# Kernel tuning notes

Measured on AMD Instinct MI355X. Metric: run time of the kernel, lower is better.

## Reference

```python
import jax, jax.numpy as jnp
import numpy as np

B, L, D, H = 4, 1024, 1024, 16
DK = D // H


def setup_inputs() -> dict:
    key = jax.random.key(0)
    ks = jax.random.split(key, 5)
    s = 1.0 / np.sqrt(D)  # roughly nn.Linear init scale
    return {
        "x": jax.random.normal(ks[0], (B, L, D), dtype=jnp.float32),
        "Wq": jax.random.normal(ks[1], (D, D), dtype=jnp.float32) * s,
        "bq": jnp.zeros((D,), dtype=jnp.float32),
        "Wk": jax.random.normal(ks[2], (D, D), dtype=jnp.float32) * s,
        "bk": jnp.zeros((D,), dtype=jnp.float32),
        "Wv": jax.random.normal(ks[3], (D, D), dtype=jnp.float32) * s,
        "bv": jnp.zeros((D,), dtype=jnp.float32),
        "Wo": jax.random.normal(ks[4], (D, D), dtype=jnp.float32) * s,
        "bo": jnp.zeros((D,), dtype=jnp.float32),
    }


def reference(x, Wq, bq, Wk, bk, Wv, bv, Wo, bo):
    b, l, d = x.shape
    # torch Linear: y = x @ W.T + b
    q = (x @ Wq.T + bq).reshape(b, l, H, DK).transpose(0, 2, 1, 3)  # [B,H,L,DK]
    k = (x @ Wk.T + bk).reshape(b, l, H, DK).transpose(0, 2, 1, 3)
    v = (x @ Wv.T + bv).reshape(b, l, H, DK).transpose(0, 2, 1, 3)
    scores = jnp.einsum("bhqd,bhkd->bhqk", q, k) / jnp.sqrt(jnp.float32(DK))
    attn = jax.nn.softmax(scores, axis=-1)  # dropout p=0 -> identity
    head_out = jnp.einsum("bhqk,bhkd->bhqd", attn, v)  # [B,H,L,DK]
    merged = head_out.transpose(0, 2, 1, 3).reshape(b, l, d)  # [B,L,D]
    out = merged @ Wo.T + bo
    # DeCov loss over head outputs
    U = merged.reshape(b * l, d)
    U = U - U.mean(axis=0, keepdims=True)
    C = (U.T @ U) / jnp.float32(b * l)
    decov = 0.5 * (jnp.sum(C * C) - jnp.sum(jnp.diag(C) ** 2))
    return (out, decov)
```

## Files before the change

### kernel.cpp

```cpp
#include <hip/hip_runtime.h>
#include <cstdint>
#include <cstddef>

typedef short v4s __attribute__((ext_vector_type(4)));
typedef short v8s __attribute__((ext_vector_type(8)));
typedef float v4f __attribute__((ext_vector_type(4)));

__device__ __forceinline__ short f2bf(float f) {
    union { float f; unsigned u; } x; x.f = f;
    unsigned r = (x.u + 0x7FFFu + ((x.u >> 16) & 1u)) >> 16;
    return (short)(unsigned short)r;
}
__device__ __forceinline__ float bf2f(short h) {
    union { unsigned u; float f; } x; x.u = ((unsigned)(unsigned short)h) << 16;
    return x.f;
}

__device__ __forceinline__ void gld16(const void* g, void* l) {
    __builtin_amdgcn_global_load_lds((const __attribute__((address_space(1))) void*)g,
                                     (__attribute__((address_space(3))) void*)l, 16, 0, 0);
}

__global__ __launch_bounds__(256) void cvt_bf16(
    const float* __restrict__ x, const float* __restrict__ wq, const float* __restrict__ wk,
    const float* __restrict__ wv, const float* __restrict__ wo,
    short* __restrict__ xb, short* __restrict__ wqb, short* __restrict__ wkb,
    short* __restrict__ wvb, short* __restrict__ wob, float* __restrict__ colsum,
    float* __restrict__ dtot, int* __restrict__ dcnt)
{
    int bid = blockIdx.x;
    const float* src; short* dst; size_t base;
    if (bid < 4096)      { src = x;  dst = xb;  base = (size_t)bid * 1024; }
    else if (bid < 5120) { src = wq; dst = wqb; base = (size_t)(bid - 4096) * 1024; }
    else if (bid < 6144) { src = wk; dst = wkb; base = (size_t)(bid - 5120) * 1024; }
    else if (bid < 7168) { src = wv; dst = wvb; base = (size_t)(bid - 6144) * 1024; }
    else                 { src = wo; dst = wob; base = (size_t)(bid - 7168) * 1024; }
    size_t idx = base + (size_t)threadIdx.x * 4;
    v4f v = *(const v4f*)(src + idx);
    v4s o;
    o[0] = f2bf(v[0]); o[1] = f2bf(v[1]); o[2] = f2bf(v[2]); o[3] = f2bf(v[3]);
    *(v4s*)(dst + idx) = o;
    if (bid == 0) {
        v4f z = {0.f, 0.f, 0.f, 0.f};
        *(v4f*)(colsum + (size_t)threadIdx.x * 4) = z;
        if (threadIdx.x == 0) { *dtot = 0.f; *dcnt = 0; }
    }
}

__global__ __launch_bounds__(256) void gemm_qkv(
    const short* __restrict__ xb,
    const short* __restrict__ wq, const short* __restrict__ wk, const short* __restrict__ wv,
    const float* __restrict__ bq, const float* __restrict__ bk, const float* __restrict__ bv,
    short* __restrict__ qo, short* __restrict__ ko, short* __restrict__ vto)
{
    __shared__ __align__(16) short At[128 * 32];
    __shared__ __align__(16) short Bt[128 * 32];
    const int K = 1024;
    const int mode = blockIdx.z;
    const short* W = (mode == 0) ? wq : (mode == 1) ? wk : wv;
    const float* bias = (mode == 0) ? bq : (mode == 1) ? bk : bv;
    const int m0 = blockIdx.y * 128, n0 = blockIdx.x * 128;
    const int tid = threadIdx.x, wave = tid >> 6, lane = tid & 63;
    const int quad = lane >> 4, ll = lane & 15;
    const int wr = wave >> 1, wc = wave & 1;
    const v4f zero4 = {0.f, 0.f, 0.f, 0.f};
    v4f acc[4][4];
    for (int i = 0; i < 4; ++i) for (int j = 0; j < 4; ++j) acc[i][j] = zero4;

    for (int k0 = 0; k0 < K; k0 += 32) {
        __syncthreads();
#pragma unroll
        for (int c = 0; c < 2; ++c) {
            int chb = (wave * 2 + c) * 64;
            int ch = chb + lane;
            int row = ch >> 2, col8 = (ch & 3) * 8;
            gld16(xb + (size_t)(m0 + row) * K + k0 + col8, &At[chb * 8]);
            gld16(W  + (size_t)(n0 + row) * K + k0 + col8, &Bt[chb * 8]);
        }
        __syncthreads();
        v8s af[4], bfr[4];
#pragma unroll
        for (int i = 0; i < 4; ++i) af[i]  = *(const v8s*)&At[(wr * 64 + i * 16 + ll) * 32 + quad * 8];
#pragma unroll
        for (int j = 0; j < 4; ++j) bfr[j] = *(const v8s*)&Bt[(wc * 64 + j * 16 + ll) * 32 + quad * 8];
#pragma unroll
        for (int i = 0; i < 4; ++i)
#pragma unroll
            for (int j = 0; j < 4; ++j)
                acc[i][j] = __builtin_amdgcn_mfma_f32_16x16x32_bf16(af[i], bfr[j], acc[i][j], 0, 0, 0);
    }

    const float scale = (mode == 0) ? 0.125f : 1.0f;
#pragma unroll
    for (int j = 0; j < 4; ++j) {
        int n = n0 + wc * 64 + j * 16 + ll;
        float bb = bias[n];
        int hh = n >> 6, dk = n & 63;
#pragma unroll
        for (int i = 0; i < 4; ++i) {
            int mbase = m0 + wr * 64 + i * 16 + quad * 4;
#pragma unroll
            for (int r = 0; r < 4; ++r) {
                int m = mbase + r;
                int b = m >> 10, li = m & 1023;
                short h = f2bf((acc[i][j][r] + bb) * scale);
                if (mode == 0)
                    qo[(((size_t)(b * 16 + hh) * 1024 + li) << 6) + dk] = h;
                else if (mode == 1)
                    ko[(((size_t)(b * 16 + hh) * 1024 + li) << 6) + dk] = h;
                else
                    vto[(((size_t)(b * 16 + hh) * 64 + dk) << 10) + li] = h;
            }
        }
    }
}

__global__ __launch_bounds__(256) void attn_flash(
    const short* __restrict__ qb, const short* __restrict__ kb, const short* __restrict__ vtb,
    float* __restrict__ merged, short* __restrict__ mergedh, float* __restrict__ colsum)
{
    __shared__ __align__(16) short Kt[64 * 64];
    __shared__ __align__(16) short Vt[64 * 64];
    __shared__ __align__(16) short Pt[4 * 32 * 68];
    const int bh = blockIdx.y, qt = blockIdx.x;
    const int tid = threadIdx.x, wave = tid >> 6, lane = tid & 63;
    const int quad = lane >> 4, ll = lane & 15;
    const short* qp = qb  + (size_t)bh * 1024 * 64;
    const short* kp = kb  + (size_t)bh * 1024 * 64;
    const short* vp = vtb + (size_t)bh * 64 * 1024;

    v8s qa[2][2];
#pragma unroll
    for (int mi = 0; mi < 2; ++mi) {
        int qrow = qt * 128 + wave * 32 + mi * 16 + ll;
        qa[mi][0] = *(const v8s*)(qp + (size_t)qrow * 64 + quad * 8);
        qa[mi][1] = *(const v8s*)(qp + (size_t)qrow * 64 + 32 + quad * 8);
    }

    const v4f zero4 = {0.f, 0.f, 0.f, 0.f};
    v4f oacc[2][4];
    for (int mi = 0; mi < 2; ++mi) for (int nt = 0; nt < 4; ++nt) oacc[mi][nt] = zero4;
    float lsum[2][4];
    for (int mi = 0; mi < 2; ++mi) for (int r = 0; r < 4; ++r) lsum[mi][r] = 0.f;
    short* pw = &Pt[wave * 32 * 68];

    for (int jt = 0; jt < 16; ++jt) {
        __syncthreads();
#pragma unroll
        for (int c = 0; c < 2; ++c) {
            int chb = (wave * 2 + c) * 64;
            int ch = chb + lane;
            int row = ch >> 3;
            int gi = ((ch & 7) ^ (row & 7)) * 8;
            gld16(kp + (size_t)(jt * 64 + row) * 64 + gi, &Kt[chb * 8]);
            gld16(vp + (size_t)row * 1024 + jt * 64 + gi, &Vt[chb * 8]);
        }
        __syncthreads();

        v4f sacc[2][4];
#pragma unroll
        for (int nt = 0; nt < 4; ++nt) {
            int n = nt * 16 + ll;
            int g0 = (quad ^ (n & 7)) * 8;
            int g1 = ((4 + quad) ^ (n & 7)) * 8;
            v8s b0 = *(const v8s*)&Kt[n * 64 + g0];
            v8s b1 = *(const v8s*)&Kt[n * 64 + g1];
#pragma unroll
            for (int mi = 0; mi < 2; ++mi) {
                v4f s = zero4;
                s = __builtin_amdgcn_mfma_f32_16x16x32_bf16(qa[mi][0], b0, s, 0, 0, 0);
                s = __builtin_amdgcn_mfma_f32_16x16x32_bf16(qa[mi][1], b1, s, 0, 0, 0);
                sacc[mi][nt] = s;
            }
        }
#pragma unroll
        for (int mi = 0; mi < 2; ++mi)
#pragma unroll
            for (int nt = 0; nt < 4; ++nt)
#pragma unroll
                for (int r = 0; r < 4; ++r) {
                    float e = __expf(sacc[mi][nt][r]);
                    lsum[mi][r] += e;
                    pw[(mi * 16 + quad * 4 + r) * 68 + nt * 16 + ll] = f2bf(e);
                }
        v8s pa[2][2];
#pragma unroll
        for (int mi = 0; mi < 2; ++mi) {
            v4s p00 = *(const v4s*)&pw[(mi * 16 + ll) * 68 + quad * 8];
            v4s p01 = *(const v4s*)&pw[(mi * 16 + ll) * 68 + quad * 8 + 4];
            v4s p10 = *(const v4s*)&pw[(mi * 16 + ll) * 68 + 32 + quad * 8];
            v4s p11 = *(const v4s*)&pw[(mi * 16 + ll) * 68 + 32 + quad * 8 + 4];
            pa[mi][0] = __builtin_shufflevector(p00, p01, 0, 1, 2, 3, 4, 5, 6, 7);
            pa[mi][1] = __builtin_shufflevector(p10, p11, 0, 1, 2, 3, 4, 5, 6, 7);
        }
#pragma unroll
        for (int nt = 0; nt < 4; ++nt) {
            int n = nt * 16 + ll;
            int g0 = (quad ^ (n & 7)) * 8;
            int g1 = ((4 + quad) ^ (n & 7)) * 8;
            v8s v0 = *(const v8s*)&Vt[n * 64 + g0];
            v8s v1 = *(const v8s*)&Vt[n * 64 + g1];
#pragma unroll
            for (int mi = 0; mi < 2; ++mi) {
                oacc[mi][nt] = __builtin_amdgcn_mfma_f32_16x16x32_bf16(pa[mi][0], v0, oacc[mi][nt], 0, 0, 0);
                oacc[mi][nt] = __builtin_amdgcn_mfma_f32_16x16x32_bf16(pa[mi][1], v1, oacc[mi][nt], 0, 0, 0);
            }
        }
    }

    const int b = bh >> 4, h = bh & 15;
    float csum[4] = {0.f, 0.f, 0.f, 0.f};
#pragma unroll
    for (int mi = 0; mi < 2; ++mi) {
        float linv[4];
#pragma unroll
        for (int r = 0; r < 4; ++r) {
            float s = lsum[mi][r];
            s += __shfl_xor(s, 1); s += __shfl_xor(s, 2);
            s += __shfl_xor(s, 4); s += __shfl_xor(s, 8);
            linv[r] = 1.0f / s;
        }
#pragma unroll
        for (int r = 0; r < 4; ++r) {
            int li = qt * 128 + wave * 32 + mi * 16 + quad * 4 + r;
            size_t rowoff = ((size_t)(b * 1024 + li)) * 1024 + h * 64;
#pragma unroll
            for (int nt = 0; nt < 4; ++nt) {
                int d = nt * 16 + ll;
                float v = oacc[mi][nt][r] * linv[r];
                merged[rowoff + d] = v;
                mergedh[rowoff + d] = f2bf(v);
                csum[nt] += v;
            }
        }
    }
#pragma unroll
    for (int nt = 0; nt < 4; ++nt) {
        csum[nt] += __shfl_xor(csum[nt], 16);
        csum[nt] += __shfl_xor(csum[nt], 32);
    }
    if (quad == 0) {
#pragma unroll
        for (int nt = 0; nt < 4; ++nt)
            atomicAdd(&colsum[h * 64 + nt * 16 + ll], csum[nt]);
    }
}

__global__ __launch_bounds__(256) void post_attn(
    const short* __restrict__ A, const short* __restrict__ W, const float* __restrict__ bias,
    float* __restrict__ out,
    const float* __restrict__ merged, const float* __restrict__ colsum,
    short* __restrict__ uth, short* __restrict__ utl)
{
    __shared__ __align__(16) char smem[18432];
    const int bid = blockIdx.x;
    const int tid = threadIdx.x;
    if (bid < 256) {
        short* At = (short*)smem;
        short* Bt = (short*)(smem + 8192);
        const int K = 1024;
        const int n0 = (bid & 7) * 128, m0 = (bid >> 3) * 128;
        const int wave = tid >> 6, lane = tid & 63;
        const int quad = lane >> 4, ll = lane & 15;
        const int wr = wave >> 1, wc = wave & 1;
        const v4f zero4 = {0.f, 0.f, 0.f, 0.f};
        v4f acc[4][4];
        for (int i = 0; i < 4; ++i) for (int j = 0; j < 4; ++j) acc[i][j] = zero4;

        for (int k0 = 0; k0 < K; k0 += 32) {
            __syncthreads();
#pragma unroll
            for (int c = 0; c < 2; ++c) {
                int chb = (wave * 2 + c) * 64;
                int ch = chb + lane;
                int row = ch >> 2, col8 = (ch & 3) * 8;
                gld16(A + (size_t)(m0 + row) * K + k0 + col8, &At[chb * 8]);
                gld16(W + (size_t)(n0 + row) * K + k0 + col8, &Bt[chb * 8]);
            }
            __syncthreads();
            v8s af[4], bfr[4];
#pragma unroll
            for (int i = 0; i < 4; ++i) af[i]  = *(const v8s*)&At[(wr * 64 + i * 16 + ll) * 32 + quad * 8];
#pragma unroll
            for (int j = 0; j < 4; ++j) bfr[j] = *(const v8s*)&Bt[(wc * 64 + j * 16 + ll) * 32 + quad * 8];
#pragma unroll
            for (int i = 0; i < 4; ++i)
#pragma unroll
                for (int j = 0; j < 4; ++j)
                    acc[i][j] = __builtin_amdgcn_mfma_f32_16x16x32_bf16(af[i], bfr[j], acc[i][j], 0, 0, 0);
        }

#pragma unroll
        for (int j = 0; j < 4; ++j) {
            int n = n0 + wc * 64 + j * 16 + ll;
            float bb = bias[n];
#pragma unroll
            for (int i = 0; i < 4; ++i) {
                int mbase = m0 + wr * 64 + i * 16 + quad * 4;
#pragma unroll
                for (int r = 0; r < 4; ++r) {
                    int m = mbase + r;
                    out[(size_t)m * 1024 + n] = acc[i][j][r] + bb;
                }
            }
        }
    } else {
        short (*Hh)[72] = (short(*)[72])smem;
        short (*Hl)[72] = (short(*)[72])(smem + 9216);
        const int cid = bid - 256;
        const int d0 = (cid & 15) * 64, m0 = (cid >> 4) * 64;
        const int r0 = tid >> 4, c4 = (tid & 15) * 4;
        float mu[4];
#pragma unroll
        for (int e = 0; e < 4; ++e) mu[e] = colsum[d0 + c4 + e] * (1.0f / 4096.0f);
        for (int rr = 0; rr < 64; rr += 16) {
            int m = m0 + rr + r0;
            v4f v = *(const v4f*)(merged + (size_t)m * 1024 + d0 + c4);
#pragma unroll
            for (int e = 0; e < 4; ++e) {
                float u = v[e] - mu[e];
                short h = f2bf(u);
                Hh[c4 + e][rr + r0] = h;
                Hl[c4 + e][rr + r0] = f2bf(u - bf2f(h));
            }
        }
        __syncthreads();
        const int d = tid >> 2, mg = (tid & 3) * 16;
        v8s a0, a1, b0, b1;
#pragma unroll
        for (int e = 0; e < 8; ++e) {
            a0[e] = Hh[d][mg + e]; a1[e] = Hh[d][mg + 8 + e];
            b0[e] = Hl[d][mg + e]; b1[e] = Hl[d][mg + 8 + e];
        }
        size_t off = (size_t)(d0 + d) * 4096 + m0 + mg;
        *(v8s*)(uth + off) = a0; *(v8s*)(uth + off + 8) = a1;
        *(v8s*)(utl + off) = b0; *(v8s*)(utl + off + 8) = b1;
    }
}

__global__ __launch_bounds__(256) void gemm_decov(
    const short* __restrict__ uth, const short* __restrict__ utl, float* __restrict__ cpart)
{
    int p = blockIdx.x, I = 0, rem = p;
    while (rem >= 8 - I) { rem -= 8 - I; ++I; }
    const int J = I + rem;
    const int kbase = blockIdx.y * 256;
    __shared__ __align__(16) short Ah[128 * 32], Al[128 * 32], Bh[128 * 32], Bl[128 * 32];
    const int tid = threadIdx.x;
    const int wave = tid >> 6, lane = tid & 63;
    const int quad = lane >> 4, ll = lane & 15;
    const int wr = wave >> 1, wc = wave & 1;
    const v4f zero4 = {0.f, 0.f, 0.f, 0.f};
    v4f acc[4][4];
    for (int i = 0; i < 4; ++i) for (int j = 0; j < 4; ++j) acc[i][j] = zero4;

    short* sarr = (wave == 0) ? Ah : (wave == 1) ? Al : (wave == 2) ? Bh : Bl;
    const short* gsrc = (wave & 1) ? utl : uth;
    const int rbase = ((wave < 2) ? I : J) * 128;
    const int srow = lane >> 2, scol = (lane & 3) * 8;

    for (int kk = 0; kk < 256; kk += 32) {
        int k0 = kbase + kk;
        __syncthreads();
#pragma unroll
        for (int c = 0; c < 8; ++c) {
            int row = c * 16 + srow;
            gld16(gsrc + (size_t)(rbase + row) * 4096 + k0 + scol, &sarr[c * 512]);
        }
        __syncthreads();
        v8s bh[4], bl[4];
#pragma unroll
        for (int j = 0; j < 4; ++j) {
            int ro = (wc * 64 + j * 16 + ll) * 32 + quad * 8;
            bh[j] = *(const v8s*)&Bh[ro];
            bl[j] = *(const v8s*)&Bl[ro];
        }
#pragma unroll
        for (int i = 0; i < 4; ++i) {
            int ro = (wr * 64 + i * 16 + ll) * 32 + quad * 8;
            v8s ah = *(const v8s*)&Ah[ro];
            v8s al = *(const v8s*)&Al[ro];
#pragma unroll
            for (int j = 0; j < 4; ++j) {
                acc[i][j] = __builtin_amdgcn_mfma_f32_16x16x32_bf16(ah, bh[j], acc[i][j], 0, 0, 0);
                acc[i][j] = __builtin_amdgcn_mfma_f32_16x16x32_bf16(ah, bl[j], acc[i][j], 0, 0, 0);
                acc[i][j] = __builtin_amdgcn_mfma_f32_16x16x32_bf16(al, bh[j], acc[i][j], 0, 0, 0);
            }
        }
    }

    float* dst = cpart + ((size_t)blockIdx.y * 36 + p) * 16384;
#pragma unroll
    for (int i = 0; i < 4; ++i)
#pragma unroll
        for (int j = 0; j < 4; ++j)
#pragma unroll
            for (int r = 0; r < 4; ++r) {
                int gi2 = wr * 64 + i * 16 + quad * 4 + r;
                int gj2 = wc * 64 + j * 16 + ll;
                dst[gi2 * 128 + gj2] = acc[i][j][r];
            }
}

__global__ __launch_bounds__(256) void decov_reduce(
    const float* __restrict__ cpart, float* __restrict__ dtot, int* __restrict__ dcnt,
    float* __restrict__ out)
{
    int p = blockIdx.x, I = 0, rem = p;
    while (rem >= 8 - I) { rem -= 8 - I; ++I; }
    const int J = I + rem;
    const int t = threadIdx.x;
    const int ebase = blockIdx.y * 4096;
    __shared__ float wsums[4];
    float s = 0.f;
#pragma unroll
    for (int it = 0; it < 4; ++it) {
        int e4 = ebase + it * 1024 + t * 4;
        v4f c = {0.f, 0.f, 0.f, 0.f};
#pragma unroll
        for (int kc = 0; kc < 16; ++kc)
            c += *(const v4f*)&cpart[((size_t)kc * 36 + p) * 16384 + e4];
        int gi = I * 128 + (e4 >> 7), colb = J * 128 + (e4 & 127);
#pragma unroll
        for (int k = 0; k < 4; ++k) {
            float cv = c[k];
            if (gi != colb + k) s += cv * cv;
        }
    }
    if (I < J) s *= 2.f;
    s += __shfl_xor(s, 1); s += __shfl_xor(s, 2); s += __shfl_xor(s, 4);
    s += __shfl_xor(s, 8); s += __shfl_xor(s, 16); s += __shfl_xor(s, 32);
    if ((t & 63) == 0) wsums[t >> 6] = s;
    __syncthreads();
    if (t == 0) {
        float blk = wsums[0] + wsums[1] + wsums[2] + wsums[3];
        float o = atomicAdd(dtot, blk);
        int old = atomicAdd(dcnt, 1 + (int)(o * 0.0f));
        if (old == 143) {
            float tot = atomicAdd(dtot, 0.0f);
            out[4194304] = 0.5f * tot / (4096.0f * 4096.0f);
        }
    }
}

extern "C" void kernel_launch(void* const* d_in, const int* in_sizes, int n_in,
                              void* d_out, int out_size, void* d_ws, size_t ws_size,
                              hipStream_t stream) {
    const float* x  = (const float*)d_in[0];
    const float* Wq = (const float*)d_in[1];
    const float* bq = (const float*)d_in[2];
    const float* Wk = (const float*)d_in[3];
    const float* bk = (const float*)d_in[4];
    const float* Wv = (const float*)d_in[5];
    const float* bv = (const float*)d_in[6];
    const float* Wo = (const float*)d_in[7];
    const float* bo = (const float*)d_in[8];
    float* out = (float*)d_out;
    char* ws = (char*)d_ws;
    const size_t MB = 1ull << 20;
    short* xb      = (short*)(ws);
    short* wqb     = (short*)(ws + 8  * MB);
    short* wkb     = (short*)(ws + 10 * MB);
    short* wvb     = (short*)(ws + 12 * MB);
    short* wob     = (short*)(ws + 14 * MB);
    short* qb      = (short*)(ws + 16 * MB);
    short* kb      = (short*)(ws + 24 * MB);
    short* vtb     = (short*)(ws + 32 * MB);
    float* merged  = (float*)(ws + 40 * MB);
    short* mergedh = (short*)(ws + 56 * MB);
    short* uth     = (short*)(ws + 65 * MB);
    short* utl     = (short*)(ws + 73 * MB);
    float* dtot    = (float*)(ws + 81 * MB);
    int*   dcnt    = (int*)(ws + 81 * MB + 64);
    float* colsum  = (float*)(ws + 81 * MB + 4096);
    float* cpart   = (float*)(ws);

    hipLaunchKernelGGL(cvt_bf16, dim3(8192), dim3(256), 0, stream,
                       x, Wq, Wk, Wv, Wo, xb, wqb, wkb, wvb, wob, colsum, dtot, dcnt);
    hipLaunchKernelGGL(gemm_qkv, dim3(8, 32, 3), dim3(256), 0, stream,
                       xb, wqb, wkb, wvb, bq, bk, bv, qb, kb, vtb);
    hipLaunchKernelGGL(attn_flash, dim3(8, 64), dim3(256), 0, stream,
                       qb, kb, vtb, merged, mergedh, colsum);
    hipLaunchKernelGGL(post_attn, dim3(1280), dim3(256), 0, stream,
                       mergedh, wob, bo, out, merged, colsum, uth, utl);
    hipLaunchKernelGGL(gemm_decov, dim3(36, 16), dim3(256), 0, stream, uth, utl, cpart);
    hipLaunchKernelGGL(decov_reduce, dim3(36, 4), dim3(256), 0, stream, cpart, dtot, dcnt, out);
}
```

Measured before the change: 241.0 us.

## Load two K/V tiles per barrier pair, use exp2, and swap attention grid order

The attention kernel now stages two 64-key K/V tiles per iteration, which halves the number of __syncthreads pairs and issues more global loads before each wait. The log2(e) factor is folded into the Q scale in the QKV GEMM so the softmax can call exp2f instead of __expf. The grid axes are swapped so consecutive blocks cover different heads rather than different query tiles of the same head, which changes L2 locality. Shared memory use doubles for K/V, which may reduce occupancy.

New measurement: 239.2 us. No clear change (-0.7%).

```diff
diff --git a/kernel.cpp b/kernel.cpp
--- a/kernel.cpp
+++ b/kernel.cpp
@@ -90,7 +90,7 @@
                 acc[i][j] = __builtin_amdgcn_mfma_f32_16x16x32_bf16(af[i], bfr[j], acc[i][j], 0, 0, 0);
     }
 
-    const float scale = (mode == 0) ? 0.125f : 1.0f;
+    const float scale = (mode == 0) ? 0.125f * 1.44269504f : 1.0f;
 #pragma unroll
     for (int j = 0; j < 4; ++j) {
         int n = n0 + wc * 64 + j * 16 + ll;
@@ -119,10 +119,10 @@
     const short* __restrict__ qb, const short* __restrict__ kb, const short* __restrict__ vtb,
     float* __restrict__ merged, short* __restrict__ mergedh, float* __restrict__ colsum)
 {
-    __shared__ __align__(16) short Kt[64 * 64];
-    __shared__ __align__(16) short Vt[64 * 64];
+    __shared__ __align__(16) short Kt[2 * 64 * 64];
+    __shared__ __align__(16) short Vt[2 * 64 * 64];
     __shared__ __align__(16) short Pt[4 * 32 * 68];
-    const int bh = blockIdx.y, qt = blockIdx.x;
+    const int bh = blockIdx.x, qt = blockIdx.y;
     const int tid = threadIdx.x, wave = tid >> 6, lane = tid & 63;
     const int quad = lane >> 4, ll = lane & 15;
     const short* qp = qb  + (size_t)bh * 1024 * 64;
@@ -144,66 +144,75 @@
     for (int mi = 0; mi < 2; ++mi) for (int r = 0; r < 4; ++r) lsum[mi][r] = 0.f;
     short* pw = &Pt[wave * 32 * 68];
 
-    for (int jt = 0; jt < 16; ++jt) {
-        __syncthreads();
-#pragma unroll
-        for (int c = 0; c < 2; ++c) {
-            int chb = (wave * 2 + c) * 64;
-            int ch = chb + lane;
-            int row = ch >> 3;
-            int gi = ((ch & 7) ^ (row & 7)) * 8;
-            gld16(kp + (size_t)(jt * 64 + row) * 64 + gi, &Kt[chb * 8]);
-            gld16(vp + (size_t)row * 1024 + jt * 64 + gi, &Vt[chb * 8]);
-        }
-        __syncthreads();
-
-        v4f sacc[2][4];
-#pragma unroll
-        for (int nt = 0; nt < 4; ++nt) {
-            int n = nt * 16 + ll;
-            int g0 = (quad ^ (n & 7)) * 8;
-            int g1 = ((4 + quad) ^ (n & 7)) * 8;
-            v8s b0 = *(const v8s*)&Kt[n * 64 + g0];
-            v8s b1 = *(const v8s*)&Kt[n * 64 + g1];
+    for (int jt2 = 0; jt2 < 8; ++jt2) {
+        __syncthreads();
+#pragma unroll
+        for (int half = 0; half < 2; ++half) {
+            int jt = jt2 * 2 + half;
+#pragma unroll
+            for (int c = 0; c < 2; ++c) {
+                int chb = (wave * 2 + c) * 64;
+                int ch = chb + lane;
+                int row = ch >> 3;
+                int gi = ((ch & 7) ^ (row & 7)) * 8;
+                gld16(kp + (size_t)(jt * 64 + row) * 64 + gi, &Kt[half * 4096 + chb * 8]);
+                gld16(vp + (size_t)row * 1024 + jt * 64 + gi, &Vt[half * 4096 + chb * 8]);
+            }
+        }
+        __syncthreads();
+
+#pragma unroll
+        for (int half = 0; half < 2; ++half) {
+            const short* Kh = &Kt[half * 4096];
+            const short* Vh = &Vt[half * 4096];
+            v4f sacc[2][4];
+#pragma unroll
+            for (int nt = 0; nt < 4; ++nt) {
+                int n = nt * 16 + ll;
+                int g0 = (quad ^ (n & 7)) * 8;
+                int g1 = ((4 + quad) ^ (n & 7)) * 8;
+                v8s b0 = *(const v8s*)&Kh[n * 64 + g0];
+                v8s b1 = *(const v8s*)&Kh[n * 64 + g1];
+#pragma unroll
+                for (int mi = 0; mi < 2; ++mi) {
+                    v4f s = zero4;
+                    s = __builtin_amdgcn_mfma_f32_16x16x32_bf16(qa[mi][0], b0, s, 0, 0, 0);
+                    s = __builtin_amdgcn_mfma_f32_16x16x32_bf16(qa[mi][1], b1, s, 0, 0, 0);
+                    sacc[mi][nt] = s;
+                }
+            }
+#pragma unroll
+            for (int mi = 0; mi < 2; ++mi)
+#pragma unroll
+                for (int nt = 0; nt < 4; ++nt)
+#pragma unroll
+                    for (int r = 0; r < 4; ++r) {
+                        float e = exp2f(sacc[mi][nt][r]);
+                        lsum[mi][r] += e;
+                        pw[(mi * 16 + quad * 4 + r) * 68 + nt * 16 + ll] = f2bf(e);
+                    }
+            v8s pa[2][2];
 #pragma unroll
             for (int mi = 0; mi < 2; ++mi) {
-                v4f s = zero4;
-                s = __builtin_amdgcn_mfma_f32_16x16x32_bf16(qa[mi][0], b0, s, 0, 0, 0);
-                s = __builtin_amdgcn_mfma_f32_16x16x32_bf16(qa[mi][1], b1, s, 0, 0, 0);
-                sacc[mi][nt] = s;
-            }
-        }
-#pragma unroll
-        for (int mi = 0; mi < 2; ++mi)
-#pragma unroll
-            for (int nt = 0; nt < 4; ++nt)
-#pragma unroll
-                for (int r = 0; r < 4; ++r) {
-                    float e = __expf(sacc[mi][nt][r]);
-                    lsum[mi][r] += e;
-                    pw[(mi * 16 + quad * 4 + r) * 68 + nt * 16 + ll] = f2bf(e);
+                v4s p00 = *(const v4s*)&pw[(mi * 16 + ll) * 68 + quad * 8];
+                v4s p01 = *(const v4s*)&pw[(mi * 16 + ll) * 68 + quad * 8 + 4];
+                v4s p10 = *(const v4s*)&pw[(mi * 16 + ll) * 68 + 32 + quad * 8];
+                v4s p11 = *(const v4s*)&pw[(mi * 16 + ll) * 68 + 32 + quad * 8 + 4];
+                pa[mi][0] = __builtin_shufflevector(p00, p01, 0, 1, 2, 3, 4, 5, 6, 7);
+                pa[mi][1] = __builtin_shufflevector(p10, p11, 0, 1, 2, 3, 4, 5, 6, 7);
+            }
+#pragma unroll
+            for (int nt = 0; nt < 4; ++nt) {
+                int n = nt * 16 + ll;
+                int g0 = (quad ^ (n & 7)) * 8;
+                int g1 = ((4 + quad) ^ (n & 7)) * 8;
+                v8s v0 = *(const v8s*)&Vh[n * 64 + g0];
+                v8s v1 = *(const v8s*)&Vh[n * 64 + g1];
+#pragma unroll
+                for (int mi = 0; mi < 2; ++mi) {
+                    oacc[mi][nt] = __builtin_amdgcn_mfma_f32_16x16x32_bf16(pa[mi][0], v0, oacc[mi][nt], 0, 0, 0);
+                    oacc[mi][nt] = __builtin_amdgcn_mfma_f32_16x16x32_bf16(pa[mi][1], v1, oacc[mi][nt], 0, 0, 0);
                 }
-        v8s pa[2][2];
-#pragma unroll
-        for (int mi = 0; mi < 2; ++mi) {
-            v4s p00 = *(const v4s*)&pw[(mi * 16 + ll) * 68 + quad * 8];
-            v4s p01 = *(const v4s*)&pw[(mi * 16 + ll) * 68 + quad * 8 + 4];
-            v4s p10 = *(const v4s*)&pw[(mi * 16 + ll) * 68 + 32 + quad * 8];
-            v4s p11 = *(const v4s*)&pw[(mi * 16 + ll) * 68 + 32 + quad * 8 + 4];
-            pa[mi][0] = __builtin_shufflevector(p00, p01, 0, 1, 2, 3, 4, 5, 6, 7);
-            pa[mi][1] = __builtin_shufflevector(p10, p11, 0, 1, 2, 3, 4, 5, 6, 7);
-        }
-#pragma unroll
-        for (int nt = 0; nt < 4; ++nt) {
-            int n = nt * 16 + ll;
-            int g0 = (quad ^ (n & 7)) * 8;
-            int g1 = ((4 + quad) ^ (n & 7)) * 8;
-            v8s v0 = *(const v8s*)&Vt[n * 64 + g0];
-            v8s v1 = *(const v8s*)&Vt[n * 64 + g1];
-#pragma unroll
-            for (int mi = 0; mi < 2; ++mi) {
-                oacc[mi][nt] = __builtin_amdgcn_mfma_f32_16x16x32_bf16(pa[mi][0], v0, oacc[mi][nt], 0, 0, 0);
-                oacc[mi][nt] = __builtin_amdgcn_mfma_f32_16x16x32_bf16(pa[mi][1], v1, oacc[mi][nt], 0, 0, 0);
             }
         }
     }
@@ -479,7 +488,7 @@
                        x, Wq, Wk, Wv, Wo, xb, wqb, wkb, wvb, wob, colsum, dtot, dcnt);
     hipLaunchKernelGGL(gemm_qkv, dim3(8, 32, 3), dim3(256), 0, stream,
                        xb, wqb, wkb, wvb, bq, bk, bv, qb, kb, vtb);
-    hipLaunchKernelGGL(attn_flash, dim3(8, 64), dim3(256), 0, stream,
+    hipLaunchKernelGGL(attn_flash, dim3(64, 8), dim3(256), 0, stream,
                        qb, kb, vtb, merged, mergedh, colsum);
     hipLaunchKernelGGL(post_attn, dim3(1280), dim3(256), 0, stream,
                        mergedh, wob, bo, out, merged, colsum, uth, utl);
```
